# Performance work log

Hardware: AMD Instinct MI355X
Metric: run time of the kernel (lower is better)

The kernel has to match this reference:

```python
import jax, jax.numpy as jnp
import numpy as np

B, S, HID = 2, 2048, 2048
H, KV, D = 16, 8, 128
EPS = 1e-6
MROPE = [21, 21, 22]  # half_dim=64 -> [64//3, 64//3, 64-2*(64//3)]
SCALE = D ** -0.5


def setup_inputs() -> dict:
    key = jax.random.key(0)
    ks = jax.random.split(key, 8)
    hidden_states = jax.random.normal(ks[0], (B, S, HID), jnp.float32)
    # 3D mrope cos/sin: one position grid per modality axis (use same arange positions)
    inv_freq = 1.0 / (10000.0 ** (jnp.arange(0, D, 2, dtype=jnp.float32) / D))  # [64]
    pos = jnp.arange(S, dtype=jnp.float32)
    freqs = pos[:, None] * inv_freq[None, :]                  # [S, 64]
    emb = jnp.concatenate([freqs, freqs], axis=-1)            # [S, 128]
    cos = jnp.broadcast_to(jnp.cos(emb)[None, None], (3, B, S, D)).astype(jnp.float32)
    sin = jnp.broadcast_to(jnp.sin(emb)[None, None], (3, B, S, D)).astype(jnp.float32)
    q_w = jax.random.normal(ks[1], (H * D, HID), jnp.float32) * 0.02
    k_w = jax.random.normal(ks[2], (KV * D, HID), jnp.float32) * 0.02
    v_w = jax.random.normal(ks[3], (KV * D, HID), jnp.float32) * 0.02
    o_w = jax.random.normal(ks[4], (HID, H * D), jnp.float32) * 0.02
    q_norm_w = jnp.ones((D,), jnp.float32)
    k_norm_w = jnp.ones((D,), jnp.float32)
    return dict(hidden_states=hidden_states, cos=cos, sin=sin, q_w=q_w, k_w=k_w,
                v_w=v_w, o_w=o_w, q_norm_w=q_norm_w, k_norm_w=k_norm_w)


def _rmsnorm(x, w):
    var = jnp.mean(jnp.square(x.astype(jnp.float32)), axis=-1, keepdims=True)
    return (x * jax.lax.rsqrt(var + EPS)).astype(x.dtype) * w


def _rotate_half(x):
    x1, x2 = jnp.split(x, 2, axis=-1)
    return jnp.concatenate([-x2, x1], axis=-1)


def _mrope_mix(t):
    # t: [3, B, S, D]; split last dim into mrope_section*2 chunks, pick chunk i from axis-0 index i%3
    sections = MROPE * 2
    idx = np.cumsum(sections)[:-1]
    chunks = jnp.split(t, idx, axis=-1)
    mixed = jnp.concatenate([c[i % 3] for i, c in enumerate(chunks)], axis=-1)  # [B, S, D]
    return mixed[:, None, :, :]  # unsqueeze head dim -> [B, 1, S, D]


def reference(hidden_states, cos, sin, q_w, k_w, v_w, o_w, q_norm_w, k_norm_w):
    # QKV projections -> [B, n_heads, S, D]
    q = (hidden_states @ q_w.T).reshape(B, S, H, D)
    k = (hidden_states @ k_w.T).reshape(B, S, KV, D)
    v = (hidden_states @ v_w.T).reshape(B, S, KV, D)
    q = _rmsnorm(q, q_norm_w).transpose(0, 2, 1, 3)   # [B, H, S, D]
    k = _rmsnorm(k, k_norm_w).transpose(0, 2, 1, 3)   # [B, KV, S, D]
    v = v.transpose(0, 2, 1, 3)                       # [B, KV, S, D]
    # 3D multimodal RoPE
    c = _mrope_mix(cos)
    s = _mrope_mix(sin)
    q = q * c + _rotate_half(q) * s
    k = k * c + _rotate_half(k) * s
    # GQA: repeat kv heads
    groups = H // KV
    k = jnp.repeat(k, groups, axis=1)  # [B, H, S, D]
    v = jnp.repeat(v, groups, axis=1)
    # causal SDPA (eager)
    scores = jnp.einsum('bhqd,bhkd->bhqk', q, k) * SCALE
    causal = jnp.tril(jnp.ones((S, S), bool))
    scores = jnp.where(causal[None, None], scores, jnp.finfo(scores.dtype).min)
    probs = jax.nn.softmax(scores, axis=-1)
    attn = jnp.einsum('bhqk,bhkd->bhqd', probs, v)     # [B, H, S, D]
    attn = attn.transpose(0, 2, 1, 3).reshape(B, S, H * D)
    return attn @ o_w.T
```

## Files before the change

### kernel.cpp

```cpp
#include <hip/hip_runtime.h>
#include <hip/hip_bf16.h>

typedef __attribute__((ext_vector_type(8))) short short8;
typedef __attribute__((ext_vector_type(4))) short short4v;
typedef __attribute__((ext_vector_type(4))) float f32x4;

#define B_ 2
#define S_ 2048
#define HID_ 2048
#define H_ 16
#define KV_ 8
#define D_ 128
#define SCALE_ 0.08838834764831845f

__device__ inline short f2bf(float f) {
    union { __hip_bfloat16 h; short s; } u;
    u.h = __float2bfloat16(f);
    return u.s;
}
__device__ inline float bf2f(short s) {
    union { short s; __hip_bfloat16 h; } u;
    u.s = s;
    return __bfloat162float(u.h);
}

__device__ inline void gld16(const short* g, short* l) {
    __builtin_amdgcn_global_load_lds(
        (const __attribute__((address_space(1))) unsigned int*)g,
        (__attribute__((address_space(3))) unsigned int*)l, 16, 0, 0);
}

__global__ __launch_bounds__(256) void cvt_bf16(const float* __restrict__ in,
                                                short* __restrict__ out, int n) {
    int i = (blockIdx.x * 256 + threadIdx.x) * 4;
    if (i >= n) return;
    float4 v = *(const float4*)(&in[i]);
    short4v o;
    o.x = f2bf(v.x); o.y = f2bf(v.y); o.z = f2bf(v.z); o.w = f2bf(v.w);
    *(short4v*)(&out[i]) = o;
}

__device__ inline int mrope_axis(int d) {
    int m = d & 63;
    return m < 21 ? 0 : (m < 42 ? 1 : 2);
}
__global__ __launch_bounds__(256) void mix_cs(const float* __restrict__ cosp,
                                              const float* __restrict__ sinp,
                                              float* __restrict__ cm,
                                              float* __restrict__ sm) {
    int idx = blockIdx.x * 256 + threadIdx.x;
    const size_t AX = (size_t)B_ * S_ * D_;
    int d = idx & (D_ - 1);
    size_t src = (size_t)mrope_axis(d) * AX + idx;
    cm[idx] = cosp[src];
    sm[idx] = sinp[src];
}

__global__ __launch_bounds__(256) void gemm_bt(const short* __restrict__ A,
                                               const short* __restrict__ B,
                                               float* __restrict__ C,
                                               int M, int N, int K) {
    __shared__ __align__(16) short As[128 * 32];
    __shared__ __align__(16) short Bs[128 * 32];
    int tid = threadIdx.x;
    int wave = tid >> 6, lane = tid & 63;
    int m16 = lane & 15, quad = lane >> 4;
    int wr = wave >> 1, wc = wave & 1;
    int m0 = blockIdx.y * 128, n0 = blockIdx.x * 128;
    int l4r = lane >> 2;
    int l4c = (lane & 3) * 8;
    f32x4 acc[4][4] = {};
    for (int k0 = 0; k0 < K; k0 += 32) {
        gld16(&A[(size_t)(m0 + wave * 32 + l4r) * K + k0 + l4c],      &As[(wave * 32) * 32]);
        gld16(&A[(size_t)(m0 + wave * 32 + 16 + l4r) * K + k0 + l4c], &As[(wave * 32 + 16) * 32]);
        gld16(&B[(size_t)(n0 + wave * 32 + l4r) * K + k0 + l4c],      &Bs[(wave * 32) * 32]);
        gld16(&B[(size_t)(n0 + wave * 32 + 16 + l4r) * K + k0 + l4c], &Bs[(wave * 32 + 16) * 32]);
        __syncthreads();
        short8 a[4], b[4];
#pragma unroll
        for (int i = 0; i < 4; ++i)
            a[i] = *(const short8*)(&As[(wr * 64 + i * 16 + m16) * 32 + quad * 8]);
#pragma unroll
        for (int j = 0; j < 4; ++j)
            b[j] = *(const short8*)(&Bs[(wc * 64 + j * 16 + m16) * 32 + quad * 8]);
#pragma unroll
        for (int i = 0; i < 4; ++i)
#pragma unroll
            for (int j = 0; j < 4; ++j)
                acc[i][j] = __builtin_amdgcn_mfma_f32_16x16x32_bf16(a[i], b[j], acc[i][j], 0, 0, 0);
        __syncthreads();
    }
#pragma unroll
    for (int i = 0; i < 4; ++i) {
        int row = m0 + wr * 64 + i * 16 + quad * 4;
#pragma unroll
        for (int j = 0; j < 4; ++j) {
            int col = n0 + wc * 64 + j * 16 + m16;
#pragma unroll
            for (int r = 0; r < 4; ++r)
                C[(size_t)(row + r) * N + col] = acc[i][j][r];
        }
    }
}

#define TP 136
__global__ __launch_bounds__(256) void qkv_fused(const short* __restrict__ A,
                                                 const short* __restrict__ Bw,
                                                 const float* __restrict__ qnw,
                                                 const float* __restrict__ knw,
                                                 const float* __restrict__ cm,
                                                 const float* __restrict__ sm,
                                                 short* __restrict__ Qb,
                                                 short* __restrict__ Kb,
                                                 short* __restrict__ Vb) {
    __shared__ __align__(16) char smem[36864];
    short* As = (short*)smem;
    short* Bs = (short*)(smem + 8192);
    short* T  = (short*)smem;
    float* partial = (float*)(smem + 34816);
    float* rsA     = (float*)(smem + 35840);
    const int K = HID_;
    int tid = threadIdx.x;
    int wave = tid >> 6, lane = tid & 63;
    int m16 = lane & 15, quad = lane >> 4;
    int wr = wave >> 1, wc = wave & 1;
    int m0 = blockIdx.y * 128, n0 = blockIdx.x * 128;
    int hk = blockIdx.x;
    int l4r = lane >> 2;
    int l4c = (lane & 3) * 8;
    f32x4 acc[4][4] = {};
    for (int k0 = 0; k0 < K; k0 += 32) {
        gld16(&A[(size_t)(m0 + wave * 32 + l4r) * K + k0 + l4c],       &As[(wave * 32) * 32]);
        gld16(&A[(size_t)(m0 + wave * 32 + 16 + l4r) * K + k0 + l4c],  &As[(wave * 32 + 16) * 32]);
        gld16(&Bw[(size_t)(n0 + wave * 32 + l4r) * K + k0 + l4c],      &Bs[(wave * 32) * 32]);
        gld16(&Bw[(size_t)(n0 + wave * 32 + 16 + l4r) * K + k0 + l4c], &Bs[(wave * 32 + 16) * 32]);
        __syncthreads();
        short8 a[4], b[4];
#pragma unroll
        for (int i = 0; i < 4; ++i)
            a[i] = *(const short8*)(&As[(wr * 64 + i * 16 + m16) * 32 + quad * 8]);
#pragma unroll
        for (int j = 0; j < 4; ++j)
            b[j] = *(const short8*)(&Bs[(wc * 64 + j * 16 + m16) * 32 + quad * 8]);
#pragma unroll
        for (int i = 0; i < 4; ++i)
#pragma unroll
            for (int j = 0; j < 4; ++j)
                acc[i][j] = __builtin_amdgcn_mfma_f32_16x16x32_bf16(a[i], b[j], acc[i][j], 0, 0, 0);
        __syncthreads();
    }
    int b = m0 >> 11, s0 = m0 & (S_ - 1);
    if (hk >= 24) {
        int kv = hk - 24;
#pragma unroll
        for (int i = 0; i < 4; ++i)
#pragma unroll
            for (int j = 0; j < 4; ++j) {
                short4v v4;
#pragma unroll
                for (int r = 0; r < 4; ++r) v4[r] = f2bf(acc[i][j][r]);
                *(short4v*)&T[(wc * 64 + j * 16 + m16) * TP + wr * 64 + i * 16 + quad * 4] = v4;
            }
        __syncthreads();
        size_t vb = ((size_t)(b * KV_ + kv)) * D_;
#pragma unroll
        for (int it = 0; it < 8; ++it) {
            int e = (it * 256 + tid) * 8;
            int dcol = e >> 7, srow = e & 127;
            *(short8*)&Vb[(vb + dcol) * S_ + s0 + srow] = *(const short8*)&T[dcol * TP + srow];
        }
    } else {
#pragma unroll
        for (int i = 0; i < 4; ++i)
#pragma unroll
            for (int r = 0; r < 4; ++r) {
                float t = 0.f;
#pragma unroll
                for (int j = 0; j < 4; ++j) t += acc[i][j][r] * acc[i][j][r];
#pragma unroll
                for (int msk = 8; msk >= 1; msk >>= 1) t += __shfl_xor(t, msk, 64);
                if (m16 == 0) partial[wc * 128 + wr * 64 + i * 16 + quad * 4 + r] = t;
            }
#pragma unroll
        for (int i = 0; i < 4; ++i)
#pragma unroll
            for (int j = 0; j < 4; ++j)
#pragma unroll
                for (int r = 0; r < 4; ++r)
                    T[(wr * 64 + i * 16 + quad * 4 + r) * TP + wc * 64 + j * 16 + m16] =
                        f2bf(acc[i][j][r]);
        __syncthreads();
        if (tid < 128) {
            float tot = partial[tid] + partial[128 + tid];
            rsA[tid] = rsqrtf(tot * (1.0f / 128.0f) + 1e-6f);
        }
        __syncthreads();
        const float* nw = (hk < 16) ? qnw : knw;
        short* outp = (hk < 16) ? (Qb + ((size_t)(b * H_ + hk)) * S_ * D_)
                                : (Kb + ((size_t)(b * KV_ + hk - 16)) * S_ * D_);
        size_t cmb = ((size_t)(b * S_ + s0)) * D_;
#pragma unroll
        for (int it = 0; it < 8; ++it) {
            int e = (it * 256 + tid) * 8;
            int row = e >> 7, colc = e & 127;
            int pc = colc ^ 64;
            float rs = rsA[row];
            float sg = (colc < 64) ? -1.f : 1.f;
            short8 nv = *(const short8*)&T[row * TP + colc];
            short8 pv = *(const short8*)&T[row * TP + pc];
            float4 cA = *(const float4*)&cm[cmb + (size_t)row * D_ + colc];
            float4 cB = *(const float4*)&cm[cmb + (size_t)row * D_ + colc + 4];
            float4 sA = *(const float4*)&sm[cmb + (size_t)row * D_ + colc];
            float4 sB = *(const float4*)&sm[cmb + (size_t)row * D_ + colc + 4];
            float4 wA = *(const float4*)&nw[colc];
            float4 wB = *(const float4*)&nw[colc + 4];
            float4 wpA = *(const float4*)&nw[pc];
            float4 wpB = *(const float4*)&nw[pc + 4];
            float cs[8] = {cA.x, cA.y, cA.z, cA.w, cB.x, cB.y, cB.z, cB.w};
            float sn[8] = {sA.x, sA.y, sA.z, sA.w, sB.x, sB.y, sB.z, sB.w};
            float wv[8] = {wA.x, wA.y, wA.z, wA.w, wB.x, wB.y, wB.z, wB.w};
            float wp[8] = {wpA.x, wpA.y, wpA.z, wpA.w, wpB.x, wpB.y, wpB.z, wpB.w};
            short8 o;
#pragma unroll
            for (int k = 0; k < 8; ++k) {
                float x = bf2f(nv[k]) * rs * wv[k];
                float p = bf2f(pv[k]) * rs * wp[k];
                o[k] = f2bf(x * cs[k] + sg * p * sn[k]);
            }
            *(short8*)&outp[(size_t)(s0 + row) * D_ + colc] = o;
        }
    }
}

#define KPAD 136
#define VPAD 72
__global__ __launch_bounds__(256) void attn_fa(const short* __restrict__ Qb,
                                               const short* __restrict__ Kb,
                                               const short* __restrict__ Vb,
                                               short* __restrict__ Ab) {
    __shared__ __align__(16) short Ks[64 * KPAD];
    __shared__ __align__(16) short Vs[128 * VPAD];
    __shared__ __align__(16) short Ps[4][16 * VPAD];
    int tid = threadIdx.x;
    int wave = tid >> 6, lane = tid & 63;
    int m16 = lane & 15, quad = lane >> 4;
    int bh = blockIdx.x;
    int h = bh & 15, b = bh >> 4;
    int qt = 31 - blockIdx.y;
    int kv = h >> 1;
    const short* Qp = Qb + (size_t)(b * H_ + h) * S_ * D_;
    const short* Kp = Kb + (size_t)(b * KV_ + kv) * S_ * D_;
    const short* Vp = Vb + (size_t)(b * KV_ + kv) * D_ * S_;
    int q_base = qt * 64 + wave * 16;
    int qrow = q_base + m16;
    short8 qf[4];
#pragma unroll
    for (int c = 0; c < 4; ++c)
        qf[c] = *(const short8*)(&Qp[(size_t)(q_base + m16) * D_ + c * 32 + quad * 8]);
    f32x4 o_acc[8] = {};
    float m_r = -1e30f, l_r = 0.f;
    int nchunks = qt + 1;
    for (int kc = 0; kc < nchunks; ++kc) {
        int k0 = kc * 64;
#pragma unroll
        for (int it = 0; it < 4; ++it) {
            int cc = tid + it * 256;
            int row = cc >> 4, col = (cc & 15) * 8;
            *(uint4*)(&Ks[row * KPAD + col]) = *(const uint4*)(&Kp[(size_t)(k0 + row) * D_ + col]);
        }
#pragma unroll
        for (int it = 0; it < 4; ++it) {
            int cc = tid + it * 256;
            int row = cc >> 3, col = (cc & 7) * 8;
            *(uint4*)(&Vs[row * VPAD + col]) = *(const uint4*)(&Vp[(size_t)row * S_ + k0 + col]);
        }
        __syncthreads();
        float sv[4][4];
#pragma unroll
        for (int nt = 0; nt < 4; ++nt) {
            f32x4 facc = {};
#pragma unroll
            for (int c = 0; c < 4; ++c) {
                short8 kfr = *(const short8*)(&Ks[(nt * 16 + m16) * KPAD + c * 32 + quad * 8]);
                facc = __builtin_amdgcn_mfma_f32_16x16x32_bf16(kfr, qf[c], facc, 0, 0, 0);
            }
            if (kc == qt) {
#pragma unroll
                for (int r = 0; r < 4; ++r) {
                    int key = k0 + nt * 16 + quad * 4 + r;
                    sv[nt][r] = (key <= qrow) ? facc[r] * SCALE_ : -1e30f;
                }
            } else {
#pragma unroll
                for (int r = 0; r < 4; ++r) sv[nt][r] = facc[r] * SCALE_;
            }
        }
        float mx = -1e30f;
#pragma unroll
        for (int nt = 0; nt < 4; ++nt)
#pragma unroll
            for (int r = 0; r < 4; ++r) mx = fmaxf(mx, sv[nt][r]);
        mx = fmaxf(mx, __shfl_xor(mx, 16, 64));
        mx = fmaxf(mx, __shfl_xor(mx, 32, 64));
        float m_new = fmaxf(m_r, mx);
        float alpha = __expf(m_r - m_new);
        float p[4][4], sum = 0.f;
#pragma unroll
        for (int nt = 0; nt < 4; ++nt)
#pragma unroll
            for (int r = 0; r < 4; ++r) { p[nt][r] = __expf(sv[nt][r] - m_new); sum += p[nt][r]; }
        sum += __shfl_xor(sum, 16, 64);
        sum += __shfl_xor(sum, 32, 64);
        l_r = l_r * alpha + sum;
        m_r = m_new;
#pragma unroll
        for (int j = 0; j < 8; ++j) {
            f32x4 t = o_acc[j];
#pragma unroll
            for (int r = 0; r < 4; ++r) t[r] *= alpha;
            o_acc[j] = t;
        }
#pragma unroll
        for (int nt = 0; nt < 4; ++nt) {
            short4v pk;
#pragma unroll
            for (int r = 0; r < 4; ++r) pk[r] = f2bf(p[nt][r]);
            *(short4v*)&Ps[wave][m16 * VPAD + nt * 16 + quad * 4] = pk;
        }
#pragma unroll
        for (int kk = 0; kk < 2; ++kk) {
            short8 pf = *(const short8*)(&Ps[wave][m16 * VPAD + kk * 32 + quad * 8]);
#pragma unroll
            for (int j = 0; j < 8; ++j) {
                short8 vfr = *(const short8*)(&Vs[(j * 16 + m16) * VPAD + kk * 32 + quad * 8]);
                o_acc[j] = __builtin_amdgcn_mfma_f32_16x16x32_bf16(vfr, pf, o_acc[j], 0, 0, 0);
            }
        }
        __syncthreads();
    }
    float inv_l = 1.0f / l_r;
    size_t base = ((size_t)(b * S_ + qrow)) * (H_ * D_) + h * D_;
#pragma unroll
    for (int j = 0; j < 8; ++j) {
        short4v ov;
#pragma unroll
        for (int r = 0; r < 4; ++r) ov[r] = f2bf(o_acc[j][r] * inv_l);
        *(short4v*)&Ab[base + j * 16 + quad * 4] = ov;
    }
}

extern "C" void kernel_launch(void* const* d_in, const int* in_sizes, int n_in,
                              void* d_out, int out_size, void* d_ws, size_t ws_size,
                              hipStream_t stream) {
    const float* hid  = (const float*)d_in[0];
    const float* cosp = (const float*)d_in[1];
    const float* sinp = (const float*)d_in[2];
    const float* q_w  = (const float*)d_in[3];
    const float* k_w  = (const float*)d_in[4];
    const float* v_w  = (const float*)d_in[5];
    const float* o_w  = (const float*)d_in[6];
    const float* qnw  = (const float*)d_in[7];
    const float* knw  = (const float*)d_in[8];

    char* w = (char*)d_ws;
    short* Hb    = (short*)w;  w += (size_t)4096 * 2048 * 2;
    short* Wqkv  = (short*)w;  w += (size_t)4096 * 2048 * 2;
    short* Owb   = (short*)w;  w += (size_t)2048 * 2048 * 2;
    short* Qb    = (short*)w;  w += (size_t)B_ * H_ * S_ * D_ * 2;
    short* Kb    = (short*)w;  w += (size_t)B_ * KV_ * S_ * D_ * 2;
    short* Vb    = (short*)w;  w += (size_t)B_ * KV_ * D_ * S_ * 2;
    short* Ab    = (short*)w;  w += (size_t)4096 * 2048 * 2;
    float* cos_m = (float*)w;  w += (size_t)B_ * S_ * D_ * 4;
    float* sin_m = (float*)w;  w += (size_t)B_ * S_ * D_ * 4;

    cvt_bf16<<<8192, 256, 0, stream>>>(hid, Hb, 4096 * 2048);
    cvt_bf16<<<4096, 256, 0, stream>>>(q_w, Wqkv, 2048 * 2048);
    cvt_bf16<<<2048, 256, 0, stream>>>(k_w, Wqkv + (size_t)2048 * 2048, 1024 * 2048);
    cvt_bf16<<<2048, 256, 0, stream>>>(v_w, Wqkv + (size_t)3072 * 2048, 1024 * 2048);
    cvt_bf16<<<4096, 256, 0, stream>>>(o_w, Owb, 2048 * 2048);
    mix_cs<<<2048, 256, 0, stream>>>(cosp, sinp, cos_m, sin_m);

    qkv_fused<<<dim3(32, 32), 256, 0, stream>>>(Hb, Wqkv, qnw, knw, cos_m, sin_m,
                                                Qb, Kb, Vb);

    attn_fa<<<dim3(32, 32), 256, 0, stream>>>(Qb, Kb, Vb, Ab);

    gemm_bt<<<dim3(16, 32), 256, 0, stream>>>(Ab, Owb, (float*)d_out, 4096, 2048, 2048);
}
```

Before: 377.6 us.

## Merge prep kernels, use K=64 swizzled LDS tiles in GEMMs, read V from global

Fuses the six conversion and mrope-mix launches into a single prep kernel, which removes launch overhead. Both GEMMs now stage K-tiles of 64 instead of 32 with an XOR-swizzled LDS layout, halving the number of barrier iterations and reducing LDS bank conflicts. The attention kernel drops V staging in LDS and reads V fragments straight from global memory, which saves LDS and a barrier-protected copy but risks uncoalesced, higher-latency loads.

```diff
diff --git a/kernel.cpp b/kernel.cpp
--- a/kernel.cpp
+++ b/kernel.cpp
@@ -30,64 +30,89 @@
         (__attribute__((address_space(3))) unsigned int*)l, 16, 0, 0);
 }
 
-__global__ __launch_bounds__(256) void cvt_bf16(const float* __restrict__ in,
-                                                short* __restrict__ out, int n) {
-    int i = (blockIdx.x * 256 + threadIdx.x) * 4;
-    if (i >= n) return;
-    float4 v = *(const float4*)(&in[i]);
-    short4v o;
-    o.x = f2bf(v.x); o.y = f2bf(v.y); o.z = f2bf(v.z); o.w = f2bf(v.w);
-    *(short4v*)(&out[i]) = o;
-}
-
 __device__ inline int mrope_axis(int d) {
     int m = d & 63;
     return m < 21 ? 0 : (m < 42 ? 1 : 2);
 }
-__global__ __launch_bounds__(256) void mix_cs(const float* __restrict__ cosp,
-                                              const float* __restrict__ sinp,
-                                              float* __restrict__ cm,
-                                              float* __restrict__ sm) {
-    int idx = blockIdx.x * 256 + threadIdx.x;
-    const size_t AX = (size_t)B_ * S_ * D_;
-    int d = idx & (D_ - 1);
-    size_t src = (size_t)mrope_axis(d) * AX + idx;
-    cm[idx] = cosp[src];
-    sm[idx] = sinp[src];
+__global__ __launch_bounds__(256) void prep(const float* __restrict__ hid,
+                                            const float* __restrict__ qw_,
+                                            const float* __restrict__ kw_,
+                                            const float* __restrict__ vw_,
+                                            const float* __restrict__ ow_,
+                                            const float* __restrict__ cosp,
+                                            const float* __restrict__ sinp,
+                                            short* __restrict__ Hb,
+                                            short* __restrict__ Wqkv,
+                                            short* __restrict__ Owb,
+                                            float* __restrict__ cm,
+                                            float* __restrict__ sm) {
+    int bid = blockIdx.x;
+    if (bid < 20480) {
+        const float* src; short* dst; int base;
+        if (bid < 8192)       { src = hid; dst = Hb;              base = bid; }
+        else if (bid < 12288) { src = qw_; dst = Wqkv;            base = bid - 8192; }
+        else if (bid < 14336) { src = kw_; dst = Wqkv + 4194304;  base = bid - 12288; }
+        else if (bid < 16384) { src = vw_; dst = Wqkv + 6291456;  base = bid - 14336; }
+        else                  { src = ow_; dst = Owb;             base = bid - 16384; }
+        int i = base * 1024 + threadIdx.x * 4;
+        float4 v = *(const float4*)(&src[i]);
+        short4v o;
+        o.x = f2bf(v.x); o.y = f2bf(v.y); o.z = f2bf(v.z); o.w = f2bf(v.w);
+        *(short4v*)(&dst[i]) = o;
+    } else {
+        const size_t AX = (size_t)B_ * S_ * D_;
+        int i0 = (bid - 20480) * 1024 + threadIdx.x * 4;
+#pragma unroll
+        for (int k = 0; k < 4; ++k) {
+            int idx = i0 + k;
+            int d = idx & (D_ - 1);
+            size_t src = (size_t)mrope_axis(d) * AX + idx;
+            cm[idx] = cosp[src];
+            sm[idx] = sinp[src];
+        }
+    }
 }
 
 __global__ __launch_bounds__(256) void gemm_bt(const short* __restrict__ A,
                                                const short* __restrict__ B,
                                                float* __restrict__ C,
                                                int M, int N, int K) {
-    __shared__ __align__(16) short As[128 * 32];
-    __shared__ __align__(16) short Bs[128 * 32];
+    __shared__ __align__(16) short As[128 * 64];
+    __shared__ __align__(16) short Bs[128 * 64];
     int tid = threadIdx.x;
     int wave = tid >> 6, lane = tid & 63;
     int m16 = lane & 15, quad = lane >> 4;
     int wr = wave >> 1, wc = wave & 1;
     int m0 = blockIdx.y * 128, n0 = blockIdx.x * 128;
-    int l4r = lane >> 2;
-    int l4c = (lane & 3) * 8;
+    int srow = lane >> 3;
+    int scol = ((lane & 7) ^ srow) << 3;
     f32x4 acc[4][4] = {};
-    for (int k0 = 0; k0 < K; k0 += 32) {
-        gld16(&A[(size_t)(m0 + wave * 32 + l4r) * K + k0 + l4c],      &As[(wave * 32) * 32]);
-        gld16(&A[(size_t)(m0 + wave * 32 + 16 + l4r) * K + k0 + l4c], &As[(wave * 32 + 16) * 32]);
-        gld16(&B[(size_t)(n0 + wave * 32 + l4r) * K + k0 + l4c],      &Bs[(wave * 32) * 32]);
-        gld16(&B[(size_t)(n0 + wave * 32 + 16 + l4r) * K + k0 + l4c], &Bs[(wave * 32 + 16) * 32]);
-        __syncthreads();
-        short8 a[4], b[4];
+    for (int k0 = 0; k0 < K; k0 += 64) {
+#pragma unroll
+        for (int i = 0; i < 4; ++i) {
+            gld16(&A[(size_t)(m0 + wave * 32 + i * 8 + srow) * K + k0 + scol],
+                  &As[(wave * 32 + i * 8) * 64]);
+            gld16(&B[(size_t)(n0 + wave * 32 + i * 8 + srow) * K + k0 + scol],
+                  &Bs[(wave * 32 + i * 8) * 64]);
+        }
+        __syncthreads();
+        short8 a[4][2], b[4][2];
 #pragma unroll
         for (int i = 0; i < 4; ++i)
-            a[i] = *(const short8*)(&As[(wr * 64 + i * 16 + m16) * 32 + quad * 8]);
-#pragma unroll
-        for (int j = 0; j < 4; ++j)
-            b[j] = *(const short8*)(&Bs[(wc * 64 + j * 16 + m16) * 32 + quad * 8]);
-#pragma unroll
-        for (int i = 0; i < 4; ++i)
-#pragma unroll
-            for (int j = 0; j < 4; ++j)
-                acc[i][j] = __builtin_amdgcn_mfma_f32_16x16x32_bf16(a[i], b[j], acc[i][j], 0, 0, 0);
+#pragma unroll
+            for (int kk = 0; kk < 2; ++kk) {
+                int gsw = (((kk << 2) + quad) ^ (m16 & 7)) << 3;
+                a[i][kk] = *(const short8*)(&As[(wr * 64 + i * 16 + m16) * 64 + gsw]);
+                b[i][kk] = *(const short8*)(&Bs[(wc * 64 + i * 16 + m16) * 64 + gsw]);
+            }
+#pragma unroll
+        for (int kk = 0; kk < 2; ++kk)
+#pragma unroll
+            for (int i = 0; i < 4; ++i)
+#pragma unroll
+                for (int j = 0; j < 4; ++j)
+                    acc[i][j] = __builtin_amdgcn_mfma_f32_16x16x32_bf16(a[i][kk], b[j][kk],
+                                                                        acc[i][j], 0, 0, 0);
         __syncthreads();
     }
 #pragma unroll
@@ -115,7 +140,7 @@
                                                  short* __restrict__ Vb) {
     __shared__ __align__(16) char smem[36864];
     short* As = (short*)smem;
-    short* Bs = (short*)(smem + 8192);
+    short* Bs = (short*)(smem + 16384);
     short* T  = (short*)smem;
     float* partial = (float*)(smem + 34816);
     float* rsA     = (float*)(smem + 35840);
@@ -126,27 +151,35 @@
     int wr = wave >> 1, wc = wave & 1;
     int m0 = blockIdx.y * 128, n0 = blockIdx.x * 128;
     int hk = blockIdx.x;
-    int l4r = lane >> 2;
-    int l4c = (lane & 3) * 8;
+    int srow = lane >> 3;
+    int scol = ((lane & 7) ^ srow) << 3;
     f32x4 acc[4][4] = {};
-    for (int k0 = 0; k0 < K; k0 += 32) {
-        gld16(&A[(size_t)(m0 + wave * 32 + l4r) * K + k0 + l4c],       &As[(wave * 32) * 32]);
-        gld16(&A[(size_t)(m0 + wave * 32 + 16 + l4r) * K + k0 + l4c],  &As[(wave * 32 + 16) * 32]);
-        gld16(&Bw[(size_t)(n0 + wave * 32 + l4r) * K + k0 + l4c],      &Bs[(wave * 32) * 32]);
-        gld16(&Bw[(size_t)(n0 + wave * 32 + 16 + l4r) * K + k0 + l4c], &Bs[(wave * 32 + 16) * 32]);
-        __syncthreads();
-        short8 a[4], b[4];
+    for (int k0 = 0; k0 < K; k0 += 64) {
+#pragma unroll
+        for (int i = 0; i < 4; ++i) {
+            gld16(&A[(size_t)(m0 + wave * 32 + i * 8 + srow) * K + k0 + scol],
+                  &As[(wave * 32 + i * 8) * 64]);
+            gld16(&Bw[(size_t)(n0 + wave * 32 + i * 8 + srow) * K + k0 + scol],
+                  &Bs[(wave * 32 + i * 8) * 64]);
+        }
+        __syncthreads();
+        short8 a[4][2], b[4][2];
 #pragma unroll
         for (int i = 0; i < 4; ++i)
-            a[i] = *(const short8*)(&As[(wr * 64 + i * 16 + m16) * 32 + quad * 8]);
-#pragma unroll
-        for (int j = 0; j < 4; ++j)
-            b[j] = *(const short8*)(&Bs[(wc * 64 + j * 16 + m16) * 32 + quad * 8]);
-#pragma unroll
-        for (int i = 0; i < 4; ++i)
-#pragma unroll
-            for (int j = 0; j < 4; ++j)
-                acc[i][j] = __builtin_amdgcn_mfma_f32_16x16x32_bf16(a[i], b[j], acc[i][j], 0, 0, 0);
+#pragma unroll
+            for (int kk = 0; kk < 2; ++kk) {
+                int gsw = (((kk << 2) + quad) ^ (m16 & 7)) << 3;
+                a[i][kk] = *(const short8*)(&As[(wr * 64 + i * 16 + m16) * 64 + gsw]);
+                b[i][kk] = *(const short8*)(&Bs[(wc * 64 + i * 16 + m16) * 64 + gsw]);
+            }
+#pragma unroll
+        for (int kk = 0; kk < 2; ++kk)
+#pragma unroll
+            for (int i = 0; i < 4; ++i)
+#pragma unroll
+                for (int j = 0; j < 4; ++j)
+                    acc[i][j] = __builtin_amdgcn_mfma_f32_16x16x32_bf16(a[i][kk], b[j][kk],
+                                                                        acc[i][j], 0, 0, 0);
         __syncthreads();
     }
     int b = m0 >> 11, s0 = m0 & (S_ - 1);
@@ -166,8 +199,8 @@
 #pragma unroll
         for (int it = 0; it < 8; ++it) {
             int e = (it * 256 + tid) * 8;
-            int dcol = e >> 7, srow = e & 127;
-            *(short8*)&Vb[(vb + dcol) * S_ + s0 + srow] = *(const short8*)&T[dcol * TP + srow];
+            int dcol = e >> 7, srw = e & 127;
+            *(short8*)&Vb[(vb + dcol) * S_ + s0 + srw] = *(const short8*)&T[dcol * TP + srw];
         }
     } else {
 #pragma unroll
@@ -239,7 +272,6 @@
                                                const short* __restrict__ Vb,
                                                short* __restrict__ Ab) {
     __shared__ __align__(16) short Ks[64 * KPAD];
-    __shared__ __align__(16) short Vs[128 * VPAD];
     __shared__ __align__(16) short Ps[4][16 * VPAD];
     int tid = threadIdx.x;
     int wave = tid >> 6, lane = tid & 63;
@@ -268,12 +300,6 @@
             int row = cc >> 4, col = (cc & 15) * 8;
             *(uint4*)(&Ks[row * KPAD + col]) = *(const uint4*)(&Kp[(size_t)(k0 + row) * D_ + col]);
         }
-#pragma unroll
-        for (int it = 0; it < 4; ++it) {
-            int cc = tid + it * 256;
-            int row = cc >> 3, col = (cc & 7) * 8;
-            *(uint4*)(&Vs[row * VPAD + col]) = *(const uint4*)(&Vp[(size_t)row * S_ + k0 + col]);
-        }
         __syncthreads();
         float sv[4][4];
 #pragma unroll
@@ -332,7 +358,7 @@
             short8 pf = *(const short8*)(&Ps[wave][m16 * VPAD + kk * 32 + quad * 8]);
 #pragma unroll
             for (int j = 0; j < 8; ++j) {
-                short8 vfr = *(const short8*)(&Vs[(j * 16 + m16) * VPAD + kk * 32 + quad * 8]);
+                short8 vfr = *(const short8*)(&Vp[(size_t)(j * 16 + m16) * S_ + k0 + kk * 32 + quad * 8]);
                 o_acc[j] = __builtin_amdgcn_mfma_f32_16x16x32_bf16(vfr, pf, o_acc[j], 0, 0, 0);
             }
         }
@@ -373,12 +399,8 @@
     float* cos_m = (float*)w;  w += (size_t)B_ * S_ * D_ * 4;
     float* sin_m = (float*)w;  w += (size_t)B_ * S_ * D_ * 4;
 
-    cvt_bf16<<<8192, 256, 0, stream>>>(hid, Hb, 4096 * 2048);
-    cvt_bf16<<<4096, 256, 0, stream>>>(q_w, Wqkv, 2048 * 2048);
-    cvt_bf16<<<2048, 256, 0, stream>>>(k_w, Wqkv + (size_t)2048 * 2048, 1024 * 2048);
-    cvt_bf16<<<2048, 256, 0, stream>>>(v_w, Wqkv + (size_t)3072 * 2048, 1024 * 2048);
-    cvt_bf16<<<4096, 256, 0, stream>>>(o_w, Owb, 2048 * 2048);
-    mix_cs<<<2048, 256, 0, stream>>>(cosp, sinp, cos_m, sin_m);
+    prep<<<20992, 256, 0, stream>>>(hid, q_w, k_w, v_w, o_w, cosp, sinp,
+                                    Hb, Wqkv, Owb, cos_m, sin_m);
 
     qkv_fused<<<dim3(32, 32), 256, 0, stream>>>(Hb, Wqkv, qnw, knw, cos_m, sin_m,
                                                 Qb, Kb, Vb);
```

After: 462.6 us. 1.23x slower.
